# Kernel tuning notes

Hardware: AMD Instinct MI355X
Metric: run time of the kernel (lower is better)

## Reference

```python
import jax, jax.numpy as jnp
import numpy as np

PI = np.pi

def setup_inputs() -> dict:
    key = jax.random.key(0)
    ks = jax.random.split(key, 8)
    N, D, K, Q = 8192, 8, 64, 16
    return {
        "X": jax.random.normal(ks[0], (N, D), dtype=jnp.float32),
        "z": jax.random.normal(ks[1], (D, K, Q), dtype=jnp.float32),
        "weight": jax.random.uniform(ks[2], (Q,), dtype=jnp.float32) + 0.5,
        "mu": jax.random.uniform(ks[3], (D, Q), dtype=jnp.float32) + 0.5,
        "std": jax.random.uniform(ks[4], (D, Q), dtype=jnp.float32) + 0.5,
        "alpha": jax.random.uniform(ks[5], (K, Q), dtype=jnp.float32) * PI,
        "var_mu_w": 0.5 * jax.random.uniform(ks[6], (D, K, Q), dtype=jnp.float32),
        "var_sigma_w": 0.05 * jax.random.uniform(ks[7], (D, K, Q), dtype=jnp.float32),
    }

def reference(X, z, weight, mu, std, alpha, var_mu_w, var_sigma_w):
    # Faithful translation of vssgp.get_Ephi (Param.transform treated as identity)
    N, D = X.shape
    _, K, Q = z.shape
    two_over_K = 2.0 * weight[None, None, :] / K                 # [1,1,Q]
    mean_p = 1.0 / (mu + 1e-8)                                   # [D,Q]
    std_p = 1.0 / (2.0 * PI * std + 1e-8)                        # [D,Q]
    E_w = mean_p[:, None, :] + std_p[:, None, :] * var_mu_w      # [D,K,Q]
    xbar = 2.0 * PI * (X[:, :, None, None] - z[None])            # [N,D,K,Q]
    phase = jnp.einsum('ndkq,dkq->nkq', xbar, E_w)               # D-reduction
    cos_w = jnp.cos(alpha[None] + phase)                         # [N,K,Q]
    decay = jnp.exp(-0.5 * jnp.einsum(
        'ndkq,dkq->nkq', (std_p[None, :, None, :] * xbar) ** 2, var_sigma_w))
    E_phi = (jnp.sqrt(two_over_K) * decay * cos_w).reshape(N, K * Q)
    cos_2w = jnp.cos(2.0 * alpha[None] + 2.0 * phase)
    E_cos_sq = two_over_K * (0.5 + 0.5 * decay ** 4 * cos_2w)    # [N,K,Q]
    G = E_phi.T @ E_phi                                          # [KQ,KQ]
    diag_new = E_cos_sq.sum(axis=0).reshape(-1)
    G = G - jnp.diag(jnp.diag(G)) + jnp.diag(diag_new)
    return E_phi, G, E_cos_sq
```

## Files before the change

### kernel.cpp

```cpp
#include <hip/hip_runtime.h>

#define TWO_PI 6.2831853071795864769f

typedef float floatx4 __attribute__((ext_vector_type(4)));
typedef float f32x16 __attribute__((ext_vector_type(16)));
typedef __bf16 bf16x8 __attribute__((ext_vector_type(8)));

__device__ __forceinline__ unsigned short f32_to_bf16(float f) {
    unsigned int u = __float_as_uint(f);
    u += 0x7fffu + ((u >> 16) & 1u);
    return (unsigned short)(u >> 16);
}

__device__ __forceinline__ void gload_lds16(const void* g, void* l) {
    __builtin_amdgcn_global_load_lds(
        (__attribute__((address_space(1))) unsigned int*)g,
        (__attribute__((address_space(3))) unsigned int*)l, 16, 0, 0);
}

__global__ __launch_bounds__(256) void k_precompute(
    const float* __restrict__ z, const float* __restrict__ weight,
    const float* __restrict__ mu, const float* __restrict__ stdv,
    const float* __restrict__ alpha, const float* __restrict__ vmw,
    const float* __restrict__ vsw, float* __restrict__ coef)
{
    int kq = blockIdx.x * blockDim.x + threadIdx.x;
    if (kq >= 1024) return;
    int q = kq & 15;
    float w = weight[q];
    float t2k = w * (2.0f / 64.0f);
    float* c = coef + (size_t)kq * 32;
#pragma unroll
    for (int d = 0; d < 8; ++d) {
        float m = mu[d * 16 + q];
        float s = stdv[d * 16 + q];
        float mean_p = 1.0f / (m + 1e-8f);
        float std_p  = 1.0f / (TWO_PI * s + 1e-8f);
        float Ew  = mean_p + std_p * vmw[d * 1024 + kq];
        float sp2 = std_p * TWO_PI;
        c[d]      = TWO_PI * Ew;
        c[8 + d]  = sp2 * sp2 * vsw[d * 1024 + kq];
        c[16 + d] = z[d * 1024 + kq];
    }
    c[24] = alpha[kq];
    c[25] = sqrtf(t2k);
    c[26] = t2k;
}

__global__ __launch_bounds__(256) void k_ephi(
    const float* __restrict__ X, const float* __restrict__ coef,
    float* __restrict__ Ephi, float* __restrict__ Ecos,
    unsigned short* __restrict__ ET, float* __restrict__ part,
    int N, int NB)
{
    __shared__ float Xs[64][8];
    __shared__ unsigned short Ebf[64][66];
    __shared__ float red[256];

    const int tid = threadIdx.x;
    const int kq0 = blockIdx.x * 64;
    const int n0  = blockIdx.y * 64;

    for (int i = tid; i < 512; i += 256)
        Xs[i >> 3][i & 7] = X[(size_t)(n0 + (i >> 3)) * 8 + (i & 7)];
    __syncthreads();

    const int kql = tid & 63;
    const int kq  = kq0 + kql;
    const int nb  = (tid >> 6) * 16;

    const float* c = coef + (size_t)kq * 32;
    float Ac[8], u[8], zv[8];
    *(floatx4*)&Ac[0] = *(const floatx4*)(c + 0);
    *(floatx4*)&Ac[4] = *(const floatx4*)(c + 4);
    *(floatx4*)&u[0]  = *(const floatx4*)(c + 8);
    *(floatx4*)&u[4]  = *(const floatx4*)(c + 12);
    *(floatx4*)&zv[0] = *(const floatx4*)(c + 16);
    *(floatx4*)&zv[4] = *(const floatx4*)(c + 20);
    const float alp = c[24], sqw = c[25], t2k = c[26];

    float csum = 0.0f;
#pragma unroll 4
    for (int nl = 0; nl < 16; ++nl) {
        const int n = nb + nl;
        floatx4 xa = *(const floatx4*)&Xs[n][0];
        floatx4 xb = *(const floatx4*)&Xs[n][4];
        float ph = 0.0f, s = 0.0f;
#pragma unroll
        for (int d = 0; d < 4; ++d) {
            float t = xa[d] - zv[d];
            ph = fmaf(Ac[d], t, ph);
            s  = fmaf(u[d], t * t, s);
        }
#pragma unroll
        for (int d = 0; d < 4; ++d) {
            float t = xb[d] - zv[4 + d];
            ph = fmaf(Ac[4 + d], t, ph);
            s  = fmaf(u[4 + d], t * t, s);
        }
        float cw  = __cosf(alp + ph);
        float dec = __expf(-0.5f * s);
        float ep  = sqw * dec * cw;
        float d2  = dec * dec;
        float c2w = fmaf(2.0f * cw, cw, -1.0f);
        float ec  = t2k * fmaf(0.5f * d2 * d2, c2w, 0.5f);
        csum += ec;
        size_t idx = (size_t)(n0 + n) * 1024 + kq;
        __builtin_nontemporal_store(ep, &Ephi[idx]);
        __builtin_nontemporal_store(ec, &Ecos[idx]);
        Ebf[kql][n] = f32_to_bf16(ep);
    }
    red[tid] = csum;
    __syncthreads();
    if (tid < 64) {
        float v = red[tid] + red[tid + 64] + red[tid + 128] + red[tid + 192];
        part[(size_t)(kq0 + tid) * NB + blockIdx.y] = v;
    }

    const int rw = tid >> 3;
    const int cw8 = tid & 7;
#pragma unroll
    for (int cc = 0; cc < 2; ++cc) {
        const int row = rw + cc * 32;
        const unsigned short* s8 = &Ebf[row][cw8 * 8];
        uint4 v;
        v.x = (unsigned)s8[0] | ((unsigned)s8[1] << 16);
        v.y = (unsigned)s8[2] | ((unsigned)s8[3] << 16);
        v.z = (unsigned)s8[4] | ((unsigned)s8[5] << 16);
        v.w = (unsigned)s8[6] | ((unsigned)s8[7] << 16);
        *(uint4*)&ET[(size_t)(kq0 + row) * N + n0 + cw8 * 8] = v;
    }
}

__global__ __launch_bounds__(256) void k_gemm(
    const unsigned short* __restrict__ ET, float* __restrict__ Gpart,
    int N, int KQ)
{
    __shared__ unsigned short At[2][128 * 64];
    __shared__ unsigned short Bt[2][128 * 64];

    const int tid  = threadIdx.x;
    const int wave = tid >> 6, lane = tid & 63;
    const int wi = wave >> 1, wj = wave & 1;

    const int bid = blockIdx.x;
    const int zc  = bid & 7;
    const int t8  = bid >> 3;
    const int i0  = (t8 >> 3) * 128;
    const int j0  = (t8 & 7) * 128;
    const int NS = N >> 3;
    const int nbase = zc * NS;
    const int nsteps = NS >> 6;

    const int srow = tid >> 3;
    const int sch  = (tid & 7) ^ (srow & 7);
    const size_t gA = (size_t)(i0 + srow) * N + nbase + sch * 8;
    const size_t gB = (size_t)(j0 + srow) * N + nbase + sch * 8;

    f32x16 acc[2][2] = {};

    auto STAGE = [&](int buf, int noff) {
        unsigned short* la = &At[buf][wave * 512];
        unsigned short* lb = &Bt[buf][wave * 512];
#pragma unroll
        for (int b = 0; b < 4; ++b) {
            gload_lds16(ET + gA + (size_t)(b * 32) * N + noff, la + b * 2048);
            gload_lds16(ET + gB + (size_t)(b * 32) * N + noff, lb + b * 2048);
        }
    };

    STAGE(0, 0);
    asm volatile("s_waitcnt vmcnt(0)" ::: "memory");
    __syncthreads();

    for (int t = 0; t < nsteps; ++t) {
        const int buf = t & 1;
        if (t + 1 < nsteps) STAGE(buf ^ 1, (t + 1) * 64);

        const unsigned short* Ab = &At[buf][0];
        const unsigned short* Bb = &Bt[buf][0];
        bf16x8 a[2][4], b[2][4];
#pragma unroll
        for (int m = 0; m < 2; ++m) {
            const int r = wi * 64 + m * 32 + (lane & 31);
#pragma unroll
            for (int ks = 0; ks < 4; ++ks) {
                const int ch = (ks * 2 + (lane >> 5)) ^ (r & 7);
                a[m][ks] = *(const bf16x8*)&Ab[r * 64 + ch * 8];
            }
        }
#pragma unroll
        for (int n = 0; n < 2; ++n) {
            const int r = wj * 64 + n * 32 + (lane & 31);
#pragma unroll
            for (int ks = 0; ks < 4; ++ks) {
                const int ch = (ks * 2 + (lane >> 5)) ^ (r & 7);
                b[n][ks] = *(const bf16x8*)&Bb[r * 64 + ch * 8];
            }
        }
#pragma unroll
        for (int ks = 0; ks < 4; ++ks)
#pragma unroll
            for (int m = 0; m < 2; ++m)
#pragma unroll
                for (int n = 0; n < 2; ++n)
                    acc[m][n] = __builtin_amdgcn_mfma_f32_32x32x16_bf16(
                        a[m][ks], b[n][ks], acc[m][n], 0, 0, 0);

        asm volatile("s_waitcnt vmcnt(0)" ::: "memory");
        __syncthreads();
    }

    float* Gp = Gpart + (size_t)zc * KQ * KQ;
    const int colb = j0 + wj * 64 + (lane & 31);
    const int rowb = i0 + wi * 64 + 4 * (lane >> 5);
#pragma unroll
    for (int m = 0; m < 2; ++m)
#pragma unroll
        for (int n = 0; n < 2; ++n)
#pragma unroll
            for (int reg = 0; reg < 16; ++reg) {
                const int row = rowb + m * 32 + (reg & 3) + 8 * (reg >> 2);
                Gp[(size_t)row * KQ + colb + n * 32] = acc[m][n][reg];
            }
}

__global__ __launch_bounds__(256) void k_reduce(
    const float* __restrict__ Gpart, const float* __restrict__ part,
    float* __restrict__ G, int KQ, int NB)
{
    const size_t off = ((size_t)blockIdx.x * 256 + threadIdx.x) * 4;
    const size_t stride = (size_t)KQ * KQ;
    floatx4 s = *(const floatx4*)&Gpart[off];
#pragma unroll
    for (int z = 1; z < 8; ++z)
        s += *(const floatx4*)&Gpart[(size_t)z * stride + off];
    const int row = (int)(off / (size_t)KQ);
    const int c0  = (int)(off % (size_t)KQ);
    if (row >= c0 && row < c0 + 4) {
        const floatx4* p = (const floatx4*)&part[(size_t)row * NB];
        floatx4 a4 = p[0];
        for (int i = 1; i < (NB >> 2); ++i) a4 += p[i];
        s[row - c0] = a4[0] + a4[1] + a4[2] + a4[3];
    }
    *(floatx4*)&G[off] = s;
}

extern "C" void kernel_launch(void* const* d_in, const int* in_sizes, int n_in,
                              void* d_out, int out_size, void* d_ws, size_t ws_size,
                              hipStream_t stream)
{
    (void)n_in; (void)out_size; (void)ws_size;
    const float* X      = (const float*)d_in[0];
    const float* z      = (const float*)d_in[1];
    const float* weight = (const float*)d_in[2];
    const float* mu     = (const float*)d_in[3];
    const float* stdv   = (const float*)d_in[4];
    const float* alpha  = (const float*)d_in[5];
    const float* vmw    = (const float*)d_in[6];
    const float* vsw    = (const float*)d_in[7];

    const int N  = in_sizes[0] / 8;
    const int KQ = in_sizes[5];
    const int NB = N / 64;

    unsigned short* ET = (unsigned short*)d_ws;
    float* Gpart = (float*)((char*)d_ws + (size_t)KQ * N * 2);
    float* part  = (float*)((char*)d_ws + (size_t)KQ * N * 2
                            + 8ull * KQ * KQ * 4);
    float* coef  = (float*)((char*)d_ws + (size_t)KQ * N * 2
                            + 8ull * KQ * KQ * 4 + (size_t)KQ * NB * 4);

    float* Ephi = (float*)d_out;
    float* G    = Ephi + (size_t)N * KQ;
    float* Ecos = G + (size_t)KQ * KQ;

    k_precompute<<<4, 256, 0, stream>>>(z, weight, mu, stdv, alpha, vmw, vsw, coef);
    k_ephi<<<dim3(KQ / 64, NB), 256, 0, stream>>>(
        X, coef, Ephi, Ecos, ET, part, N, NB);
    k_gemm<<<512, 256, 0, stream>>>(ET, Gpart, N, KQ);
    k_reduce<<<(KQ * KQ) / 1024, 256, 0, stream>>>(Gpart, part, G, KQ, NB);
}
```

Measured before the change: 140.6 us.

## Compute only upper-triangular Gram tiles and mirror them in the reduce kernel

```diff
diff --git a/kernel.cpp b/kernel.cpp
--- a/kernel.cpp
+++ b/kernel.cpp
@@ -54,7 +54,7 @@
     int N, int NB)
 {
     __shared__ float Xs[64][8];
-    __shared__ unsigned short Ebf[64][66];
+    __shared__ unsigned Ebu[64][36];
     __shared__ float red[256];
 
     const int tid = threadIdx.x;
@@ -80,7 +80,9 @@
     const float alp = c[24], sqw = c[25], t2k = c[26];
 
     float csum = 0.0f;
-#pragma unroll 4
+    unsigned pk[8];
+    unsigned short prevb = 0;
+#pragma unroll
     for (int nl = 0; nl < 16; ++nl) {
         const int n = nb + nl;
         floatx4 xa = *(const floatx4*)&Xs[n][0];
@@ -108,7 +110,16 @@
         size_t idx = (size_t)(n0 + n) * 1024 + kq;
         __builtin_nontemporal_store(ep, &Ephi[idx]);
         __builtin_nontemporal_store(ec, &Ecos[idx]);
-        Ebf[kql][n] = f32_to_bf16(ep);
+        unsigned short b = f32_to_bf16(ep);
+        if (nl & 1) pk[nl >> 1] = (unsigned)prevb | ((unsigned)b << 16);
+        else        prevb = b;
+    }
+    {
+        const int nb2 = nb >> 1;
+        uint4 v0 = { pk[0], pk[1], pk[2], pk[3] };
+        uint4 v1 = { pk[4], pk[5], pk[6], pk[7] };
+        *(uint4*)&Ebu[kql][nb2]     = v0;
+        *(uint4*)&Ebu[kql][nb2 + 4] = v1;
     }
     red[tid] = csum;
     __syncthreads();
@@ -117,24 +128,18 @@
         part[(size_t)(kq0 + tid) * NB + blockIdx.y] = v;
     }
 
-    const int rw = tid >> 3;
-    const int cw8 = tid & 7;
-#pragma unroll
-    for (int cc = 0; cc < 2; ++cc) {
-        const int row = rw + cc * 32;
-        const unsigned short* s8 = &Ebf[row][cw8 * 8];
-        uint4 v;
-        v.x = (unsigned)s8[0] | ((unsigned)s8[1] << 16);
-        v.y = (unsigned)s8[2] | ((unsigned)s8[3] << 16);
-        v.z = (unsigned)s8[4] | ((unsigned)s8[5] << 16);
-        v.w = (unsigned)s8[6] | ((unsigned)s8[7] << 16);
-        *(uint4*)&ET[(size_t)(kq0 + row) * N + n0 + cw8 * 8] = v;
-    }
+    const int r = tid >> 2;
+    const int s4 = (tid & 3) * 8;
+    uint4 w0 = *(const uint4*)&Ebu[r][s4];
+    uint4 w1 = *(const uint4*)&Ebu[r][s4 + 4];
+    uint4* dst = (uint4*)&ET[(size_t)(kq0 + r) * N + n0 + (tid & 3) * 16];
+    dst[0] = w0;
+    dst[1] = w1;
 }
 
 __global__ __launch_bounds__(256) void k_gemm(
     const unsigned short* __restrict__ ET, float* __restrict__ Gpart,
-    int N, int KQ)
+    int N, int NT)
 {
     __shared__ unsigned short At[2][128 * 64];
     __shared__ unsigned short Bt[2][128 * 64];
@@ -144,11 +149,14 @@
     const int wi = wave >> 1, wj = wave & 1;
 
     const int bid = blockIdx.x;
-    const int zc  = bid & 7;
-    const int t8  = bid >> 3;
-    const int i0  = (t8 >> 3) * 128;
-    const int j0  = (t8 & 7) * 128;
-    const int NS = N >> 3;
+    const int zc  = bid & 15;
+    const int uu  = bid >> 4;
+    int ti = 0, rem = uu;
+    while (rem >= NT - ti) { rem -= NT - ti; ++ti; }
+    const int tj = ti + rem;
+    const int i0 = ti * 128, j0 = tj * 128;
+
+    const int NS = N >> 4;
     const int nbase = zc * NS;
     const int nsteps = NS >> 6;
 
@@ -182,20 +190,20 @@
         bf16x8 a[2][4], b[2][4];
 #pragma unroll
         for (int m = 0; m < 2; ++m) {
-            const int r = wi * 64 + m * 32 + (lane & 31);
+            const int rr = wi * 64 + m * 32 + (lane & 31);
 #pragma unroll
             for (int ks = 0; ks < 4; ++ks) {
-                const int ch = (ks * 2 + (lane >> 5)) ^ (r & 7);
-                a[m][ks] = *(const bf16x8*)&Ab[r * 64 + ch * 8];
+                const int ch = (ks * 2 + (lane >> 5)) ^ (rr & 7);
+                a[m][ks] = *(const bf16x8*)&Ab[rr * 64 + ch * 8];
             }
         }
 #pragma unroll
         for (int n = 0; n < 2; ++n) {
-            const int r = wj * 64 + n * 32 + (lane & 31);
+            const int rr = wj * 64 + n * 32 + (lane & 31);
 #pragma unroll
             for (int ks = 0; ks < 4; ++ks) {
-                const int ch = (ks * 2 + (lane >> 5)) ^ (r & 7);
-                b[n][ks] = *(const bf16x8*)&Bb[r * 64 + ch * 8];
+                const int ch = (ks * 2 + (lane >> 5)) ^ (rr & 7);
+                b[n][ks] = *(const bf16x8*)&Bb[rr * 64 + ch * 8];
             }
         }
 #pragma unroll
@@ -211,9 +219,9 @@
         __syncthreads();
     }
 
-    float* Gp = Gpart + (size_t)zc * KQ * KQ;
-    const int colb = j0 + wj * 64 + (lane & 31);
-    const int rowb = i0 + wi * 64 + 4 * (lane >> 5);
+    float* Gp = Gpart + ((size_t)uu * 16 + zc) * 16384;
+    const int colb = wj * 64 + (lane & 31);
+    const int rowb = wi * 64 + 4 * (lane >> 5);
 #pragma unroll
     for (int m = 0; m < 2; ++m)
 #pragma unroll
@@ -221,29 +229,65 @@
 #pragma unroll
             for (int reg = 0; reg < 16; ++reg) {
                 const int row = rowb + m * 32 + (reg & 3) + 8 * (reg >> 2);
-                Gp[(size_t)row * KQ + colb + n * 32] = acc[m][n][reg];
+                Gp[row * 128 + colb + n * 32] = acc[m][n][reg];
             }
 }
 
 __global__ __launch_bounds__(256) void k_reduce(
     const float* __restrict__ Gpart, const float* __restrict__ part,
-    float* __restrict__ G, int KQ, int NB)
-{
-    const size_t off = ((size_t)blockIdx.x * 256 + threadIdx.x) * 4;
-    const size_t stride = (size_t)KQ * KQ;
-    floatx4 s = *(const floatx4*)&Gpart[off];
-#pragma unroll
-    for (int z = 1; z < 8; ++z)
-        s += *(const floatx4*)&Gpart[(size_t)z * stride + off];
-    const int row = (int)(off / (size_t)KQ);
-    const int c0  = (int)(off % (size_t)KQ);
-    if (row >= c0 && row < c0 + 4) {
-        const floatx4* p = (const floatx4*)&part[(size_t)row * NB];
-        floatx4 a4 = p[0];
-        for (int i = 1; i < (NB >> 2); ++i) a4 += p[i];
-        s[row - c0] = a4[0] + a4[1] + a4[2] + a4[3];
-    }
-    *(floatx4*)&G[off] = s;
+    float* __restrict__ G, int KQ, int NB, int NT)
+{
+    const int uu = blockIdx.x >> 2;
+    const int ch = blockIdx.x & 3;
+    int ti = 0, rem = uu;
+    while (rem >= NT - ti) { rem -= NT - ti; ++ti; }
+    const int tj = ti + rem;
+
+    __shared__ float T[32][132];
+
+    const int tid = threadIdx.x;
+    const size_t ub = (size_t)uu * 16 * 16384 + (size_t)ch * 4096;
+
+#pragma unroll
+    for (int i = 0; i < 4; ++i) {
+        const int lf  = tid + i * 256;
+        const int off = lf * 4;
+        floatx4 v = *(const floatx4*)&Gpart[ub + off];
+#pragma unroll
+        for (int z = 1; z < 16; ++z)
+            v += *(const floatx4*)&Gpart[ub + (size_t)z * 16384 + off];
+
+        const int rl = lf >> 5;
+        const int cl = off & 127;
+        const int gi = ti * 128 + ch * 32 + rl;
+        const int gj = tj * 128 + cl;
+        if (ti == tj && gi >= gj && gi < gj + 4) {
+            const floatx4* p = (const floatx4*)&part[(size_t)gi * NB];
+            floatx4 a4 = p[0];
+            for (int k = 1; k < (NB >> 2); ++k) a4 += p[k];
+            v[gi - gj] = a4[0] + a4[1] + a4[2] + a4[3];
+        }
+        *(floatx4*)&G[(size_t)gi * KQ + gj] = v;
+        if (ti != tj) *(floatx4*)&T[rl][cl] = v;
+    }
+
+    if (ti == tj) return;
+    __syncthreads();
+
+#pragma unroll
+    for (int i = 0; i < 4; ++i) {
+        const int lf2 = tid + i * 256;
+        const int r2 = lf2 >> 3;
+        const int c2 = (lf2 * 4) & 31;
+        floatx4 v;
+        v[0] = T[c2 + 0][r2];
+        v[1] = T[c2 + 1][r2];
+        v[2] = T[c2 + 2][r2];
+        v[3] = T[c2 + 3][r2];
+        const int gi = tj * 128 + r2;
+        const int gj = ti * 128 + ch * 32 + c2;
+        *(floatx4*)&G[(size_t)gi * KQ + gj] = v;
+    }
 }
 
 extern "C" void kernel_launch(void* const* d_in, const int* in_sizes, int n_in,
@@ -263,13 +307,14 @@
     const int N  = in_sizes[0] / 8;
     const int KQ = in_sizes[5];
     const int NB = N / 64;
-
-    unsigned short* ET = (unsigned short*)d_ws;
-    float* Gpart = (float*)((char*)d_ws + (size_t)KQ * N * 2);
-    float* part  = (float*)((char*)d_ws + (size_t)KQ * N * 2
-                            + 8ull * KQ * KQ * 4);
-    float* coef  = (float*)((char*)d_ws + (size_t)KQ * N * 2
-                            + 8ull * KQ * KQ * 4 + (size_t)KQ * NB * 4);
+    const int NT = KQ >> 7;
+    const int NU = NT * (NT + 1) / 2;
+
+    size_t o = 0;
+    unsigned short* ET = (unsigned short*)d_ws;          o += (size_t)KQ * N * 2;
+    float* Gpart = (float*)((char*)d_ws + o);            o += (size_t)NU * 16 * 16384 * 4;
+    float* part  = (float*)((char*)d_ws + o);            o += (size_t)KQ * NB * 4;
+    float* coef  = (float*)((char*)d_ws + o);
 
     float* Ephi = (float*)d_out;
     float* G    = Ephi + (size_t)N * KQ;
@@ -278,6 +323,6 @@
     k_precompute<<<4, 256, 0, stream>>>(z, weight, mu, stdv, alpha, vmw, vsw, coef);
     k_ephi<<<dim3(KQ / 64, NB), 256, 0, stream>>>(
         X, coef, Ephi, Ecos, ET, part, N, NB);
-    k_gemm<<<512, 256, 0, stream>>>(ET, Gpart, N, KQ);
-    k_reduce<<<(KQ * KQ) / 1024, 256, 0, stream>>>(Gpart, part, G, KQ, NB);
-}
+    k_gemm<<<NU * 16, 256, 0, stream>>>(ET, Gpart, N, NT);
+    k_reduce<<<NU * 4, 256, 0, stream>>>(Gpart, part, G, KQ, NB, NT);
+}
```

Result: slower. 158.7 us (+12.9%).
